# Performance work log

Measured on AMD Instinct MI355X. Metric: run time of the kernel, lower is better.

Reference implementation:

```python
import jax, jax.numpy as jnp
import numpy as np

C = 16       # cell_state_size
HID = 256    # hidden_size
L = 3        # num_layers (interim)
B, H, W = 8, 128, 128


def setup_inputs() -> dict:
    key = jax.random.key(0)
    ks = jax.random.split(key, 7)
    s = lambda *d: 1.0 / np.sqrt(d[-1])
    x = jax.random.uniform(ks[0], (B, H, W, C), dtype=jnp.float32)
    conv_w = jax.random.normal(ks[1], (C, C, 3, 3), dtype=jnp.float32) * (1.0 / np.sqrt(C * 9))
    w_first = jax.random.normal(ks[2], (HID, C), dtype=jnp.float32) * s(C)
    b_first = jax.random.normal(ks[3], (HID,), dtype=jnp.float32) * 0.01
    w_interim = jax.random.normal(ks[4], (L, HID, HID), dtype=jnp.float32) * s(HID)
    b_interim = jax.random.normal(ks[5], (L, HID), dtype=jnp.float32) * 0.01
    # NOTE: original zero-inits fcLast; we use small random so outputs/grads are nontrivial.
    w_last = jax.random.normal(ks[6], (C, HID), dtype=jnp.float32) * (0.02 * s(HID))
    return {"x": x, "conv_w": conv_w, "w_first": w_first, "b_first": b_first,
            "w_interim": w_interim, "b_interim": b_interim, "w_last": w_last,
            "steps": 16}


def _nca_step(h, conv_w, w_first, b_first, w_interim, b_interim, w_last):
    # perceive: torch does conv on x.transpose(-3,-1), i.e. [B,C,W,H]; mimic exactly.
    xt = jnp.transpose(h, (0, 3, 2, 1))  # [B,C,W,H]
    p = jax.lax.conv_general_dilated(
        xt, conv_w, window_strides=(1, 1), padding='SAME',
        dimension_numbers=('NCHW', 'OIHW', 'NCHW'))
    p = jnp.transpose(p, (0, 3, 2, 1))  # back to [B,H,W,C]
    # per-cell MLP (Linear broadcasts over B,H,W; matches flatten+view in torch)
    ds = jax.nn.relu(p @ w_first.T + b_first)
    for i in range(w_interim.shape[0]):  # small fixed layer count
        ds = jax.nn.relu(ds @ w_interim[i].T + b_interim[i])
    ds = ds @ w_last.T  # no bias
    return h + ds  # residual update (dropouts are identity in eval mode)


def reference(x, conv_w, w_first, b_first, w_interim, b_interim, w_last, steps):
    def body(h, _):
        h = _nca_step(h, conv_w, w_first, b_first, w_interim, b_interim, w_last)
        return h, h
    x_final, hist = jax.lax.scan(body, x, None, length=steps)
    history = jnp.concatenate([x[None], hist], axis=0)  # [steps+1,B,H,W,C]
    return x_final, history
```

## Files before the change

kernel.cpp:

```cpp
#include <hip/hip_runtime.h>
#include <stdint.h>
#include <stddef.h>


typedef __bf16 bf16_t;
typedef bf16_t bf16x8 __attribute__((ext_vector_type(8)));
typedef bf16_t bf16x4 __attribute__((ext_vector_type(4)));
typedef float  f32x4  __attribute__((ext_vector_type(4)));

#define N_B     8
#define N_H     128
#define N_W     128
#define N_C     16
#define HID     256
#define N_L     3
#define N_STEPS 16
#define M_TILE  128
#define THREADS 512
#define N_CELLS (N_B * N_H * N_W)
#define K1      160
#define KK1     5
#define KKH     8

__device__ __forceinline__ int swz(int row, int byteoff) {
  return byteoff ^ ((row & 7) << 4);
}

__global__ void prep_kernel(const float* __restrict__ conv_w,
                            const float* __restrict__ w_first,
                            const float* __restrict__ w_interim,
                            const float* __restrict__ w_last,
                            bf16_t* __restrict__ W1c_lin,
                            bf16_t* __restrict__ Wi_lin,
                            bf16_t* __restrict__ Wl_lin) {
  const int tid = blockIdx.x * blockDim.x + threadIdx.x;
  const int nth = gridDim.x * blockDim.x;
  for (int idx = tid; idx < 256 * K1; idx += nth) {
    int e = idx & 7, lane = (idx >> 3) & 63, nt = (idx >> 9) & 1, r = idx >> 10;
    int kk = r % KK1, wid = r / KK1;
    int col = wid * 32 + nt * 16 + (lane & 15);
    int k = kk * 32 + (lane >> 4) * 8 + e;
    float v = 0.f;
    if (k < 144) {
      int tap = k >> 4, i = k & 15;
      int dy = tap / 3 - 1, dx = tap % 3 - 1;
      for (int o = 0; o < 16; ++o)
        v += w_first[col * 16 + o] * conv_w[((o * 16 + i) * 3 + (dx + 1)) * 3 + (dy + 1)];
    }
    W1c_lin[idx] = (bf16_t)v;
  }
  for (int idx = tid; idx < N_L * HID * HID; idx += nth) {
    int l = idx / (HID * HID), idx2 = idx % (HID * HID);
    int e = idx2 & 7, lane = (idx2 >> 3) & 63, nt = (idx2 >> 9) & 1, r = idx2 >> 10;
    int kk = r & 7, wid = r >> 3;
    int col = wid * 32 + nt * 16 + (lane & 15);
    int k = kk * 32 + (lane >> 4) * 8 + e;
    Wi_lin[idx] = (bf16_t)w_interim[(l * HID + col) * HID + k];
  }
  for (int idx = tid; idx < N_C * HID; idx += nth) {
    int e = idx & 7, lane = (idx >> 3) & 63, kk = idx >> 9;
    int col = lane & 15;
    int k = kk * 32 + (lane >> 4) * 8 + e;
    Wl_lin[idx] = (bf16_t)w_last[col * HID + k];
  }
}

template <int KK>
__device__ __forceinline__ void mlp2(uint8_t* __restrict__ b0,
                                     uint8_t* __restrict__ b1,
                                     const bf16_t* __restrict__ Wlin,
                                     const float* __restrict__ bias,
                                     int lane, int wid) {
  const int lr = lane & 15;
  const int lk = lane >> 4;
  const int nbase = wid * 32;
  const bf16x8* __restrict__ wfrag = (const bf16x8*)Wlin + (wid * KK) * 2 * 64 + lane;
  f32x4 acc[2][4][2];
#pragma unroll
  for (int nt = 0; nt < 2; ++nt) {
    f32x4 binit = *(const f32x4*)(bias + nbase + nt * 16 + lk * 4);
#pragma unroll
    for (int mt = 0; mt < 4; ++mt) { acc[0][mt][nt] = binit; acc[1][mt][nt] = binit; }
  }
#pragma unroll
  for (int kk = 0; kk < KK; ++kk) {
    bf16x8 bfr[2];
#pragma unroll
    for (int nt = 0; nt < 2; ++nt) bfr[nt] = wfrag[(kk * 2 + nt) * 64];
    const int kb = kk * 64 + lk * 16;
    bf16x8 a[4];
#pragma unroll
    for (int mt = 0; mt < 4; ++mt) {
      int row = mt * 16 + lr;
      a[mt] = *(const bf16x8*)(b0 + row * 512 + swz(row, kb));
    }
#pragma unroll
    for (int mt = 0; mt < 4; ++mt)
#pragma unroll
      for (int nt = 0; nt < 2; ++nt)
        acc[0][mt][nt] = __builtin_amdgcn_mfma_f32_16x16x32_bf16(bfr[nt], a[mt], acc[0][mt][nt], 0, 0, 0);
#pragma unroll
    for (int mt = 0; mt < 4; ++mt) {
      int row = mt * 16 + lr;
      a[mt] = *(const bf16x8*)(b1 + row * 512 + swz(row, kb));
    }
#pragma unroll
    for (int mt = 0; mt < 4; ++mt)
#pragma unroll
      for (int nt = 0; nt < 2; ++nt)
        acc[1][mt][nt] = __builtin_amdgcn_mfma_f32_16x16x32_bf16(bfr[nt], a[mt], acc[1][mt][nt], 0, 0, 0);
  }
  __syncthreads();
#pragma unroll
  for (int tile = 0; tile < 2; ++tile) {
    uint8_t* tb = tile ? b1 : b0;
#pragma unroll
    for (int mt = 0; mt < 4; ++mt)
#pragma unroll
      for (int nt = 0; nt < 2; ++nt) {
        bf16x4 w;
#pragma unroll
        for (int j = 0; j < 4; ++j) w[j] = (bf16_t)fmaxf(acc[tile][mt][nt][j], 0.f);
        int row = mt * 16 + lr;
        int nb = (nbase + nt * 16 + lk * 4) * 2;
        *(bf16x4*)(tb + row * 512 + swz(row, nb)) = w;
      }
  }
}

__global__ __launch_bounds__(THREADS, 4)
void nca_step_kernel(const float* __restrict__ hsrc, float* __restrict__ hdst,
                     const bf16_t* __restrict__ W1c_lin, const bf16_t* __restrict__ Wi_lin,
                     const bf16_t* __restrict__ Wl_lin,
                     const float* __restrict__ b_first,
                     const float* __restrict__ b_interim) {
  __shared__ __align__(16) uint8_t buf[2][64 * 512];

  const int t = threadIdx.x;
  const int lane = t & 63;
  const int wid = t >> 6;
  const int by = blockIdx.x;
  const int b = by >> 7;
  const int y = by & 127;

  {
    const int m = t & 127;
    const int q = t >> 7;
    uint8_t* tb = buf[m >> 6];
    const int row = m & 63;
#pragma unroll
    for (int jj = 0; jj < 9; ++jj) {
      int k4 = q * 9 + jj;
      int tap = k4 >> 2, i0 = (k4 & 3) * 4;
      int dy = tap / 3 - 1, dx = tap % 3 - 1;
      int yy = y + dy, xx = m + dx;
      f32x4 v = {0.f, 0.f, 0.f, 0.f};
      if ((unsigned)yy < (unsigned)N_H && (unsigned)xx < (unsigned)N_W)
        v = *(const f32x4*)(hsrc + ((b * N_H + yy) * N_W + xx) * N_C + i0);
      bf16x4 w;
#pragma unroll
      for (int j = 0; j < 4; ++j) w[j] = (bf16_t)v[j];
      *(bf16x4*)(tb + row * 512 + swz(row, 8 * k4)) = w;
    }
    bf16x4 z;
#pragma unroll
    for (int j = 0; j < 4; ++j) z[j] = (bf16_t)0.f;
    int k4p = 36 + q;
    *(bf16x4*)(tb + row * 512 + swz(row, 8 * k4p)) = z;
  }
  __syncthreads();

  mlp2<KK1>(buf[0], buf[1], W1c_lin, b_first, lane, wid);
  __syncthreads();
  mlp2<KKH>(buf[0], buf[1], Wi_lin + 0 * HID * HID, b_interim + 0 * HID, lane, wid);
  __syncthreads();
  mlp2<KKH>(buf[0], buf[1], Wi_lin + 1 * HID * HID, b_interim + 1 * HID, lane, wid);
  __syncthreads();
  mlp2<KKH>(buf[0], buf[1], Wi_lin + 2 * HID * HID, b_interim + 2 * HID, lane, wid);
  __syncthreads();

  {
    const int lr = lane & 15;
    const int lk = lane >> 4;
    const uint8_t* tb = buf[wid >> 2];
    const int rb = (wid & 3) * 16;
    const bf16x8* __restrict__ wl = (const bf16x8*)Wl_lin + lane;
    f32x4 acc = {0.f, 0.f, 0.f, 0.f};
#pragma unroll
    for (int kk = 0; kk < KKH; ++kk) {
      int row = rb + lr;
      bf16x8 a = *(const bf16x8*)(tb + row * 512 + swz(row, kk * 64 + lk * 16));
      bf16x8 bb = wl[kk * 64];
      acc = __builtin_amdgcn_mfma_f32_16x16x32_bf16(bb, a, acc, 0, 0, 0);
    }
    const int cell = by * M_TILE + wid * 16 + lr;
    const int gi = cell * N_C + lk * 4;
    f32x4 r = *(const f32x4*)(hsrc + gi);
#pragma unroll
    for (int j = 0; j < 4; ++j) r[j] += acc[j];
    *(f32x4*)(hdst + gi) = r;
  }
}

extern "C" void kernel_launch(void* const* d_in, const int* in_sizes, int n_in,
                              void* d_out, int out_size, void* d_ws, size_t ws_size,
                              hipStream_t stream) {
  const float* x         = (const float*)d_in[0];
  const float* conv_w    = (const float*)d_in[1];
  const float* w_first   = (const float*)d_in[2];
  const float* b_first   = (const float*)d_in[3];
  const float* w_interim = (const float*)d_in[4];
  const float* b_interim = (const float*)d_in[5];
  const float* w_last    = (const float*)d_in[6];

  float* xfinal = (float*)d_out;
  float* hist   = xfinal + (size_t)N_CELLS * N_C;

  bf16_t* W1c_lin = (bf16_t*)d_ws;
  bf16_t* Wi_lin  = W1c_lin + 256 * K1;
  bf16_t* Wl_lin  = Wi_lin + N_L * HID * HID;

  prep_kernel<<<64, 256, 0, stream>>>(conv_w, w_first, w_interim, w_last,
                                      W1c_lin, Wi_lin, Wl_lin);
  hipMemcpyAsync(hist, x, (size_t)N_CELLS * N_C * sizeof(float),
                 hipMemcpyDeviceToDevice, stream);
  for (int s = 0; s < N_STEPS; ++s)
    nca_step_kernel<<<N_CELLS / M_TILE, THREADS, 0, stream>>>(
        hist + (size_t)s * N_CELLS * N_C, hist + (size_t)(s + 1) * N_CELLS * N_C,
        W1c_lin, Wi_lin, Wl_lin, b_first, b_interim);
  hipMemcpyAsync(xfinal, hist + (size_t)N_STEPS * N_CELLS * N_C,
                 (size_t)N_CELLS * N_C * sizeof(float),
                 hipMemcpyDeviceToDevice, stream);
}
```

Measured before the change: 1.071 ms.

## Switch MLP layers from 16x16x32 to 32x32x16 MFMA with repacked weights

Replaces the 16x16x32 bf16 MFMA tiling in the hidden MLP layers with 32x32x16 MFMA. Each wave now computes two 32x32 output tiles per 64-row buffer instead of eight 16x16 tiles, and the weight fragments are repacked in the prep kernel to match. This reduces LDS reads for the A operand and the instruction count per FLOP. It also adds s_setprio around the MFMA bursts to favour matrix issue. Accumulator register pressure is similar, but the swizzled LDS access pattern changes and may conflict differently.

```diff
diff --git a/kernel.cpp b/kernel.cpp
--- a/kernel.cpp
+++ b/kernel.cpp
@@ -7,6 +7,7 @@
 typedef bf16_t bf16x8 __attribute__((ext_vector_type(8)));
 typedef bf16_t bf16x4 __attribute__((ext_vector_type(4)));
 typedef float  f32x4  __attribute__((ext_vector_type(4)));
+typedef float  f32x16 __attribute__((ext_vector_type(16)));
 
 #define N_B     8
 #define N_H     128
@@ -19,8 +20,9 @@
 #define THREADS 512
 #define N_CELLS (N_B * N_H * N_W)
 #define K1      160
-#define KK1     5
-#define KKH     8
+#define KK1     10
+#define KKH     16
+#define KKL     8
 
 __device__ __forceinline__ int swz(int row, int byteoff) {
   return byteoff ^ ((row & 7) << 4);
@@ -36,10 +38,10 @@
   const int tid = blockIdx.x * blockDim.x + threadIdx.x;
   const int nth = gridDim.x * blockDim.x;
   for (int idx = tid; idx < 256 * K1; idx += nth) {
-    int e = idx & 7, lane = (idx >> 3) & 63, nt = (idx >> 9) & 1, r = idx >> 10;
+    int e = idx & 7, lane = (idx >> 3) & 63, r = idx >> 9;
     int kk = r % KK1, wid = r / KK1;
-    int col = wid * 32 + nt * 16 + (lane & 15);
-    int k = kk * 32 + (lane >> 4) * 8 + e;
+    int col = wid * 32 + (lane & 31);
+    int k = kk * 16 + (lane >> 5) * 8 + e;
     float v = 0.f;
     if (k < 144) {
       int tap = k >> 4, i = k & 15;
@@ -50,11 +52,11 @@
     W1c_lin[idx] = (bf16_t)v;
   }
   for (int idx = tid; idx < N_L * HID * HID; idx += nth) {
-    int l = idx / (HID * HID), idx2 = idx % (HID * HID);
-    int e = idx2 & 7, lane = (idx2 >> 3) & 63, nt = (idx2 >> 9) & 1, r = idx2 >> 10;
-    int kk = r & 7, wid = r >> 3;
-    int col = wid * 32 + nt * 16 + (lane & 15);
-    int k = kk * 32 + (lane >> 4) * 8 + e;
+    int l = idx >> 16, idx2 = idx & 65535;
+    int e = idx2 & 7, lane = (idx2 >> 3) & 63, r = idx2 >> 9;
+    int kk = r & 15, wid = r >> 4;
+    int col = wid * 32 + (lane & 31);
+    int k = kk * 16 + (lane >> 5) * 8 + e;
     Wi_lin[idx] = (bf16_t)w_interim[(l * HID + col) * HID + k];
   }
   for (int idx = tid; idx < N_C * HID; idx += nth) {
@@ -71,60 +73,52 @@
                                      const bf16_t* __restrict__ Wlin,
                                      const float* __restrict__ bias,
                                      int lane, int wid) {
-  const int lr = lane & 15;
-  const int lk = lane >> 4;
+  const int lc = lane & 31;
+  const int lh = lane >> 5;
   const int nbase = wid * 32;
-  const bf16x8* __restrict__ wfrag = (const bf16x8*)Wlin + (wid * KK) * 2 * 64 + lane;
-  f32x4 acc[2][4][2];
-#pragma unroll
-  for (int nt = 0; nt < 2; ++nt) {
-    f32x4 binit = *(const f32x4*)(bias + nbase + nt * 16 + lk * 4);
-#pragma unroll
-    for (int mt = 0; mt < 4; ++mt) { acc[0][mt][nt] = binit; acc[1][mt][nt] = binit; }
+  const bf16x8* __restrict__ wfrag = (const bf16x8*)Wlin + (wid * KK) * 64 + lane;
+  f32x16 acc[2][2];
+#pragma unroll
+  for (int q = 0; q < 4; ++q) {
+    f32x4 bq = *(const f32x4*)(bias + nbase + 8 * q + 4 * lh);
+#pragma unroll
+    for (int t = 0; t < 2; ++t)
+#pragma unroll
+      for (int m = 0; m < 2; ++m)
+#pragma unroll
+        for (int j = 0; j < 4; ++j) acc[t][m][4 * q + j] = bq[j];
   }
 #pragma unroll
   for (int kk = 0; kk < KK; ++kk) {
-    bf16x8 bfr[2];
-#pragma unroll
-    for (int nt = 0; nt < 2; ++nt) bfr[nt] = wfrag[(kk * 2 + nt) * 64];
-    const int kb = kk * 64 + lk * 16;
-    bf16x8 a[4];
-#pragma unroll
-    for (int mt = 0; mt < 4; ++mt) {
-      int row = mt * 16 + lr;
-      a[mt] = *(const bf16x8*)(b0 + row * 512 + swz(row, kb));
-    }
-#pragma unroll
-    for (int mt = 0; mt < 4; ++mt)
-#pragma unroll
-      for (int nt = 0; nt < 2; ++nt)
-        acc[0][mt][nt] = __builtin_amdgcn_mfma_f32_16x16x32_bf16(bfr[nt], a[mt], acc[0][mt][nt], 0, 0, 0);
-#pragma unroll
-    for (int mt = 0; mt < 4; ++mt) {
-      int row = mt * 16 + lr;
-      a[mt] = *(const bf16x8*)(b1 + row * 512 + swz(row, kb));
-    }
-#pragma unroll
-    for (int mt = 0; mt < 4; ++mt)
-#pragma unroll
-      for (int nt = 0; nt < 2; ++nt)
-        acc[1][mt][nt] = __builtin_amdgcn_mfma_f32_16x16x32_bf16(bfr[nt], a[mt], acc[1][mt][nt], 0, 0, 0);
-  }
-  __syncthreads();
-#pragma unroll
-  for (int tile = 0; tile < 2; ++tile) {
-    uint8_t* tb = tile ? b1 : b0;
-#pragma unroll
-    for (int mt = 0; mt < 4; ++mt)
-#pragma unroll
-      for (int nt = 0; nt < 2; ++nt) {
-        bf16x4 w;
-#pragma unroll
-        for (int j = 0; j < 4; ++j) w[j] = (bf16_t)fmaxf(acc[tile][mt][nt][j], 0.f);
-        int row = mt * 16 + lr;
-        int nb = (nbase + nt * 16 + lk * 4) * 2;
-        *(bf16x4*)(tb + row * 512 + swz(row, nb)) = w;
+    bf16x8 w = wfrag[kk * 64];
+    const int kb = kk * 32 + lh * 16;
+    bf16x8 a00 = *(const bf16x8*)(b0 + lc * 512 + swz(lc, kb));
+    bf16x8 a01 = *(const bf16x8*)(b0 + (32 + lc) * 512 + swz(32 + lc, kb));
+    bf16x8 a10 = *(const bf16x8*)(b1 + lc * 512 + swz(lc, kb));
+    bf16x8 a11 = *(const bf16x8*)(b1 + (32 + lc) * 512 + swz(32 + lc, kb));
+    __builtin_amdgcn_s_setprio(1);
+    acc[0][0] = __builtin_amdgcn_mfma_f32_32x32x16_bf16(w, a00, acc[0][0], 0, 0, 0);
+    acc[0][1] = __builtin_amdgcn_mfma_f32_32x32x16_bf16(w, a01, acc[0][1], 0, 0, 0);
+    acc[1][0] = __builtin_amdgcn_mfma_f32_32x32x16_bf16(w, a10, acc[1][0], 0, 0, 0);
+    acc[1][1] = __builtin_amdgcn_mfma_f32_32x32x16_bf16(w, a11, acc[1][1], 0, 0, 0);
+    __builtin_amdgcn_s_setprio(0);
+  }
+  __syncthreads();
+#pragma unroll
+  for (int t = 0; t < 2; ++t) {
+    uint8_t* tb = t ? b1 : b0;
+#pragma unroll
+    for (int m = 0; m < 2; ++m) {
+      int row = m * 32 + lc;
+#pragma unroll
+      for (int q = 0; q < 4; ++q) {
+        bf16x4 wv;
+#pragma unroll
+        for (int j = 0; j < 4; ++j) wv[j] = (bf16_t)fmaxf(acc[t][m][4 * q + j], 0.f);
+        int nb = (nbase + 8 * q + 4 * lh) * 2;
+        *(bf16x4*)(tb + row * 512 + swz(row, nb)) = wv;
       }
+    }
   }
 }
 
@@ -187,7 +181,7 @@
     const bf16x8* __restrict__ wl = (const bf16x8*)Wl_lin + lane;
     f32x4 acc = {0.f, 0.f, 0.f, 0.f};
 #pragma unroll
-    for (int kk = 0; kk < KKH; ++kk) {
+    for (int kk = 0; kk < KKL; ++kk) {
       int row = rb + lr;
       bf16x8 a = *(const bf16x8*)(tb + row * 512 + swz(row, kk * 64 + lk * 16));
       bf16x8 bb = wl[kk * 64];
```

Result: slower. 1.248 ms (+16.5%).
